# Optimization experiments

Measured on AMD Instinct MI355X. Metric: run time of the kernel, lower is better.

The kernel has to match this reference:

```python
import jax, jax.numpy as jnp
import numpy as np

B, N, D = 256, 131072, 256
TEMP = 0.05
EPS_SM = 1e-6
EPS_LOG = 1e-6
NUM_CLUSTERS = 1000


def _l2norm(x):
    return x / jnp.linalg.norm(x, axis=-1, keepdims=True)


def setup_inputs() -> dict:
    key = jax.random.key(0)
    k1, k2, k3, k4, k5 = jax.random.split(key, 5)
    # re-ID features are L2-normalized in practice; keeps exp(logits/temp) finite
    inputs = _l2norm(jax.random.normal(k1, (B, D), jnp.float32))
    indexes = jax.random.randint(k2, (B,), 0, N)
    labels = jax.random.randint(k3, (N,), 0, NUM_CLUSTERS)  # pseudo cluster ids buffer
    cluster_features = _l2norm(jax.random.normal(k4, (N, D), jnp.float32))
    instance_features = _l2norm(jax.random.normal(k5, (N, D), jnp.float32))
    return {
        "inputs": inputs,
        "cluster_features": cluster_features,
        "instance_features": instance_features,
        "indexes": indexes,
        "labels": labels,
    }


def reference(inputs, cluster_features, instance_features, indexes, labels):
    # targets = labels[indexes]
    targets = labels[indexes]
    # bank similarity GEMM, temperature scaling
    logits = jnp.matmul(inputs, cluster_features.T) / TEMP  # [B, N]
    # module's custom softmax: exp / (sum + eps)  (intentionally no max-subtract)
    exps = jnp.exp(logits)
    masked_sim = exps / (jnp.sum(exps, axis=1, keepdims=True) + EPS_SM)
    logp = jnp.log(masked_sim + EPS_LOG)
    # F.nll_loss: mean of -logp at target column
    loss = -jnp.mean(jnp.take_along_axis(logp, targets[:, None], axis=1))
    return loss
```

## Files before the change

### kernel.cpp

```cpp
#include <hip/hip_runtime.h>
#include <hip/hip_bf16.h>
#include <cstdint>

#define B_ 256
#define N_ 131072
#define D_ 256
#define INV_TEMP 20.0f
#define EPS_SM 1e-6f
#define EPS_LOG 1e-6f

#define TPB 512
#define BN 128
#define BK 64
#define TILES 4
#define LDB 72
#define BUFE (BN * LDB)
#define NSLOT 32
#define NBLK (N_ / (TILES * BN))

typedef __bf16 bf16_t;
typedef bf16_t bf16x8 __attribute__((ext_vector_type(8)));
typedef float f32x4 __attribute__((ext_vector_type(4)));

__device__ inline ushort f2bf(float f) {
  uint32_t u = __builtin_bit_cast(uint32_t, f);
  u += 0x7FFFu + ((u >> 16) & 1u);
  return (ushort)(u >> 16);
}

struct alignas(16) U8 { ushort u[8]; };

__global__ __launch_bounds__(TPB, 2)
void gemm_rowsum_fused(const float* __restrict__ inp, const float* __restrict__ cf,
                       const int* __restrict__ idx, const int* __restrict__ lab,
                       float* __restrict__ rowsum, unsigned* __restrict__ counter,
                       float* __restrict__ out) {
  __shared__ ushort smem[2 * BUFE];
  __shared__ unsigned done;
  const int tid  = threadIdx.x;
  const int wave = tid >> 6;
  const int lane = tid & 63;
  const int m15  = lane & 15;
  const int q    = lane >> 4;

  const size_t nbase = (size_t)blockIdx.x * (TILES * BN);
  const int brow = tid >> 2, bcg = tid & 3;
#define LDADDR(c) (cf + (nbase + (size_t)((c) >> 2) * BN + brow) * D_ + ((c) & 3) * BK + bcg * 16)

  float4 ldbuf[2][4];
#pragma unroll
  for (int i = 0; i < 4; ++i) ldbuf[0][i] = *(const float4*)(LDADDR(0) + i * 4);
#pragma unroll
  for (int i = 0; i < 4; ++i) ldbuf[1][i] = *(const float4*)(LDADDR(1) + i * 4);

  bf16x8 areg[8][2];
#pragma unroll
  for (int kc = 0; kc < 4; ++kc)
#pragma unroll
    for (int ks = 0; ks < 2; ++ks)
#pragma unroll
      for (int mb = 0; mb < 2; ++mb) {
        const float* s = inp + (wave * 32 + mb * 16 + m15) * D_ + kc * BK + ks * 32 + q * 8;
        const float4 v0 = *(const float4*)s;
        const float4 v1 = *(const float4*)(s + 4);
        U8 t;
        t.u[0] = f2bf(v0.x); t.u[1] = f2bf(v0.y); t.u[2] = f2bf(v0.z); t.u[3] = f2bf(v0.w);
        t.u[4] = f2bf(v1.x); t.u[5] = f2bf(v1.y); t.u[6] = f2bf(v1.z); t.u[7] = f2bf(v1.w);
        areg[kc * 2 + ks][mb] = __builtin_bit_cast(bf16x8, t);
      }

  f32x4 acc[2][8];
  float rs[2][4];
#pragma unroll
  for (int mb = 0; mb < 2; ++mb) {
#pragma unroll
    for (int nb = 0; nb < 8; ++nb) acc[mb][nb] = (f32x4){0.f, 0.f, 0.f, 0.f};
#pragma unroll
    for (int r = 0; r < 4; ++r) rs[mb][r] = 0.f;
  }

  {
    ushort* dst = &smem[brow * LDB + bcg * 16];
#pragma unroll
    for (int i = 0; i < 4; ++i) {
      const float4 v = ldbuf[0][i];
      U8 w;
      w.u[0] = f2bf(v.x); w.u[1] = f2bf(v.y); w.u[2] = f2bf(v.z); w.u[3] = f2bf(v.w);
      *(ushort4*)(dst + i * 4) = *(const ushort4*)&w.u[0];
    }
  }

#pragma unroll
  for (int c = 0; c < TILES * 4; ++c) {
    __syncthreads();
    if (c + 2 < TILES * 4) {
#pragma unroll
      for (int i = 0; i < 4; ++i) ldbuf[c & 1][i] = *(const float4*)(LDADDR(c + 2) + i * 4);
    }
    const ushort* bs = &smem[(c & 1) * BUFE];
#pragma unroll
    for (int ks = 0; ks < 2; ++ks) {
      bf16x8 bfr[8];
#pragma unroll
      for (int nb = 0; nb < 8; ++nb)
        bfr[nb] = __builtin_bit_cast(
            bf16x8, *(const uint4*)(&bs[(nb * 16 + m15) * LDB + ks * 32 + q * 8]));
#pragma unroll
      for (int mb = 0; mb < 2; ++mb)
#pragma unroll
        for (int nb = 0; nb < 8; ++nb)
          acc[mb][nb] = __builtin_amdgcn_mfma_f32_16x16x32_bf16(
              areg[(c & 3) * 2 + ks][mb], bfr[nb], acc[mb][nb], 0, 0, 0);
    }
    if ((c & 3) == 3) {
#pragma unroll
      for (int mb = 0; mb < 2; ++mb)
#pragma unroll
        for (int nb = 0; nb < 8; ++nb)
#pragma unroll
          for (int r = 0; r < 4; ++r)
            rs[mb][r] += __expf(acc[mb][nb][r] * INV_TEMP);
      if (c + 1 < TILES * 4) {
#pragma unroll
        for (int mb = 0; mb < 2; ++mb)
#pragma unroll
          for (int nb = 0; nb < 8; ++nb) acc[mb][nb] = (f32x4){0.f, 0.f, 0.f, 0.f};
      }
    }
    if (c + 1 < TILES * 4) {
      ushort* dst = &smem[((c + 1) & 1) * BUFE + brow * LDB + bcg * 16];
#pragma unroll
      for (int i = 0; i < 4; ++i) {
        const float4 v = ldbuf[(c + 1) & 1][i];
        U8 w;
        w.u[0] = f2bf(v.x); w.u[1] = f2bf(v.y); w.u[2] = f2bf(v.z); w.u[3] = f2bf(v.w);
        *(ushort4*)(dst + i * 4) = *(const ushort4*)&w.u[0];
      }
    }
  }

#pragma unroll
  for (int off = 8; off >= 1; off >>= 1)
#pragma unroll
    for (int mb = 0; mb < 2; ++mb)
#pragma unroll
      for (int r = 0; r < 4; ++r)
        rs[mb][r] += __shfl_xor(rs[mb][r], off, 64);

  if (m15 == 0) {
    float* slot = rowsum + (blockIdx.x & (NSLOT - 1)) * B_;
#pragma unroll
    for (int mb = 0; mb < 2; ++mb)
#pragma unroll
      for (int r = 0; r < 4; ++r)
        atomicAdd(&slot[wave * 32 + mb * 16 + q * 4 + r], rs[mb][r]);
  }
#undef LDADDR

  __syncthreads();
  if (tid == 0) {
    __threadfence();
    const unsigned prev = __hip_atomic_fetch_add(counter, 1u, __ATOMIC_ACQ_REL,
                                                 __HIP_MEMORY_SCOPE_AGENT);
    done = (prev == (unsigned)(gridDim.x - 1)) ? 1u : 0u;
  }
  __syncthreads();
  if (done) {
    __threadfence();
    float* red = (float*)smem;
    const int b = tid >> 1, part = tid & 1;
    const int t = lab[idx[b]];
    const float4* a4 = (const float4*)(inp + b * D_ + part * 128);
    const float4* c4 = (const float4*)(cf + (size_t)t * D_ + part * 128);
    float dot = 0.f;
#pragma unroll
    for (int i = 0; i < 32; ++i) {
      const float4 x = a4[i], y = c4[i];
      dot += x.x * y.x + x.y * y.y + x.z * y.z + x.w * y.w;
    }
    red[tid] = dot;
    __syncthreads();
    if (tid < 256) {
      const float d = red[2 * tid] + red[2 * tid + 1];
      float S = 0.f;
#pragma unroll
      for (int s = 0; s < NSLOT; ++s)
        S += __hip_atomic_load(&rowsum[s * B_ + tid], __ATOMIC_RELAXED,
                               __HIP_MEMORY_SCOPE_AGENT);
      red[512 + tid] = __logf(__expf(d * INV_TEMP) / (S + EPS_SM) + EPS_LOG);
    }
    __syncthreads();
    for (int off = 128; off >= 1; off >>= 1) {
      if (tid < off) red[512 + tid] += red[512 + tid + off];
      __syncthreads();
    }
    if (tid == 0) out[0] = -red[512] * (1.0f / 256.0f);
  }
}

extern "C" void kernel_launch(void* const* d_in, const int* in_sizes, int n_in,
                              void* d_out, int out_size, void* d_ws, size_t ws_size,
                              hipStream_t stream) {
  const float* inp = (const float*)d_in[0];
  const float* cf  = (const float*)d_in[1];
  const int* idx = (const int*)d_in[3];
  const int* lab = (const int*)d_in[4];
  float* out = (float*)d_out;
  float* rowsum = (float*)d_ws;
  unsigned* counter = (unsigned*)(rowsum + NSLOT * B_);

  hipMemsetAsync(d_ws, 0, (NSLOT * B_ + 16) * sizeof(float), stream);
  gemm_rowsum_fused<<<dim3(NBLK), dim3(TPB), 0, stream>>>(inp, cf, idx, lab,
                                                          rowsum, counter, out);
}
```

Before: 292.8 us.

## Shrink bank tile to 32 rows per chunk and stage input conversion via LDS

Cuts the per-chunk bank tile from 128 to 32 rows and gives each block 256 bank rows instead of 512, so the grid doubles to 512 blocks. Launch bounds rise to 4 blocks per CU, which needs the smaller accumulator footprint. The input matrix is now converted to bf16 with coalesced loads into shared memory and then read back into registers, where before each lane loaded it directly from global. The prefetch depth also changes to loads issued three chunks ahead. The aim is more occupancy and latency hiding on a memory-bound GEMM, at the cost of more barriers per unit of work, and only 4 MFMAs per ks step shared between those barriers.

```diff
diff --git a/kernel.cpp b/kernel.cpp
--- a/kernel.cpp
+++ b/kernel.cpp
@@ -10,13 +10,14 @@
 #define EPS_LOG 1e-6f
 
 #define TPB 512
-#define BN 128
+#define BROWS 256
+#define BN 32
 #define BK 64
-#define TILES 4
+#define NCHUNK 32
 #define LDB 72
 #define BUFE (BN * LDB)
 #define NSLOT 32
-#define NBLK (N_ / (TILES * BN))
+#define NBLK (N_ / BROWS)
 
 typedef __bf16 bf16_t;
 typedef bf16_t bf16x8 __attribute__((ext_vector_type(8)));
@@ -28,14 +29,12 @@
   return (ushort)(u >> 16);
 }
 
-struct alignas(16) U8 { ushort u[8]; };
-
-__global__ __launch_bounds__(TPB, 2)
+__global__ __launch_bounds__(TPB, 4)
 void gemm_rowsum_fused(const float* __restrict__ inp, const float* __restrict__ cf,
                        const int* __restrict__ idx, const int* __restrict__ lab,
                        float* __restrict__ rowsum, unsigned* __restrict__ counter,
                        float* __restrict__ out) {
-  __shared__ ushort smem[2 * BUFE];
+  __shared__ ushort smem[B_ * LDB];
   __shared__ unsigned done;
   const int tid  = threadIdx.x;
   const int wave = tid >> 6;
@@ -43,72 +42,67 @@
   const int m15  = lane & 15;
   const int q    = lane >> 4;
 
-  const size_t nbase = (size_t)blockIdx.x * (TILES * BN);
-  const int brow = tid >> 2, bcg = tid & 3;
-#define LDADDR(c) (cf + (nbase + (size_t)((c) >> 2) * BN + brow) * D_ + ((c) & 3) * BK + bcg * 16)
-
-  float4 ldbuf[2][4];
-#pragma unroll
-  for (int i = 0; i < 4; ++i) ldbuf[0][i] = *(const float4*)(LDADDR(0) + i * 4);
-#pragma unroll
-  for (int i = 0; i < 4; ++i) ldbuf[1][i] = *(const float4*)(LDADDR(1) + i * 4);
+  const size_t nbase = (size_t)blockIdx.x * BROWS;
+  const int brow = tid >> 4, bcg = tid & 15;
+#define LDADDR(c) (cf + (nbase + (size_t)((c) >> 2) * BN + brow) * D_ + ((c) & 3) * BK + bcg * 4)
+
+  float4 ldbuf[2];
+  ldbuf[0] = *(const float4*)LDADDR(0);
+  ldbuf[1] = *(const float4*)LDADDR(1);
 
   bf16x8 areg[8][2];
 #pragma unroll
-  for (int kc = 0; kc < 4; ++kc)
-#pragma unroll
-    for (int ks = 0; ks < 2; ++ks)
-#pragma unroll
-      for (int mb = 0; mb < 2; ++mb) {
-        const float* s = inp + (wave * 32 + mb * 16 + m15) * D_ + kc * BK + ks * 32 + q * 8;
-        const float4 v0 = *(const float4*)s;
-        const float4 v1 = *(const float4*)(s + 4);
-        U8 t;
-        t.u[0] = f2bf(v0.x); t.u[1] = f2bf(v0.y); t.u[2] = f2bf(v0.z); t.u[3] = f2bf(v0.w);
-        t.u[4] = f2bf(v1.x); t.u[5] = f2bf(v1.y); t.u[6] = f2bf(v1.z); t.u[7] = f2bf(v1.w);
-        areg[kc * 2 + ks][mb] = __builtin_bit_cast(bf16x8, t);
-      }
-
-  f32x4 acc[2][8];
+  for (int kc = 0; kc < 4; ++kc) {
+    const int row = tid >> 1, half = tid & 1;
+    const float* src = inp + row * D_ + kc * BK + half * 32;
+#pragma unroll
+    for (int i = 0; i < 8; ++i) {
+      const float4 v = *(const float4*)(src + i * 4);
+      ushort4 w = {f2bf(v.x), f2bf(v.y), f2bf(v.z), f2bf(v.w)};
+      *(ushort4*)(&smem[row * LDB + half * 32 + i * 4]) = w;
+    }
+    __syncthreads();
+#pragma unroll
+    for (int mb = 0; mb < 2; ++mb)
+#pragma unroll
+      for (int ks = 0; ks < 2; ++ks)
+        areg[kc * 2 + ks][mb] = __builtin_bit_cast(
+            bf16x8, *(const uint4*)(&smem[(wave * 32 + mb * 16 + m15) * LDB + ks * 32 + q * 8]));
+    __syncthreads();
+  }
+
+  f32x4 acc[2][2];
   float rs[2][4];
 #pragma unroll
   for (int mb = 0; mb < 2; ++mb) {
 #pragma unroll
-    for (int nb = 0; nb < 8; ++nb) acc[mb][nb] = (f32x4){0.f, 0.f, 0.f, 0.f};
+    for (int nb = 0; nb < 2; ++nb) acc[mb][nb] = (f32x4){0.f, 0.f, 0.f, 0.f};
 #pragma unroll
     for (int r = 0; r < 4; ++r) rs[mb][r] = 0.f;
   }
 
   {
-    ushort* dst = &smem[brow * LDB + bcg * 16];
-#pragma unroll
-    for (int i = 0; i < 4; ++i) {
-      const float4 v = ldbuf[0][i];
-      U8 w;
-      w.u[0] = f2bf(v.x); w.u[1] = f2bf(v.y); w.u[2] = f2bf(v.z); w.u[3] = f2bf(v.w);
-      *(ushort4*)(dst + i * 4) = *(const ushort4*)&w.u[0];
-    }
-  }
-
-#pragma unroll
-  for (int c = 0; c < TILES * 4; ++c) {
-    __syncthreads();
-    if (c + 2 < TILES * 4) {
-#pragma unroll
-      for (int i = 0; i < 4; ++i) ldbuf[c & 1][i] = *(const float4*)(LDADDR(c + 2) + i * 4);
-    }
+    const float4 v = ldbuf[0];
+    ushort4 w = {f2bf(v.x), f2bf(v.y), f2bf(v.z), f2bf(v.w)};
+    *(ushort4*)(&smem[brow * LDB + bcg * 4]) = w;
+  }
+  ldbuf[0] = *(const float4*)LDADDR(2);
+
+#pragma unroll
+  for (int c = 0; c < NCHUNK; ++c) {
+    __syncthreads();
     const ushort* bs = &smem[(c & 1) * BUFE];
 #pragma unroll
     for (int ks = 0; ks < 2; ++ks) {
-      bf16x8 bfr[8];
-#pragma unroll
-      for (int nb = 0; nb < 8; ++nb)
+      bf16x8 bfr[2];
+#pragma unroll
+      for (int nb = 0; nb < 2; ++nb)
         bfr[nb] = __builtin_bit_cast(
             bf16x8, *(const uint4*)(&bs[(nb * 16 + m15) * LDB + ks * 32 + q * 8]));
 #pragma unroll
       for (int mb = 0; mb < 2; ++mb)
 #pragma unroll
-        for (int nb = 0; nb < 8; ++nb)
+        for (int nb = 0; nb < 2; ++nb)
           acc[mb][nb] = __builtin_amdgcn_mfma_f32_16x16x32_bf16(
               areg[(c & 3) * 2 + ks][mb], bfr[nb], acc[mb][nb], 0, 0, 0);
     }
@@ -116,26 +110,24 @@
 #pragma unroll
       for (int mb = 0; mb < 2; ++mb)
 #pragma unroll
-        for (int nb = 0; nb < 8; ++nb)
+        for (int nb = 0; nb < 2; ++nb)
 #pragma unroll
           for (int r = 0; r < 4; ++r)
             rs[mb][r] += __expf(acc[mb][nb][r] * INV_TEMP);
-      if (c + 1 < TILES * 4) {
+      if (c + 1 < NCHUNK) {
 #pragma unroll
         for (int mb = 0; mb < 2; ++mb)
 #pragma unroll
-          for (int nb = 0; nb < 8; ++nb) acc[mb][nb] = (f32x4){0.f, 0.f, 0.f, 0.f};
+          for (int nb = 0; nb < 2; ++nb) acc[mb][nb] = (f32x4){0.f, 0.f, 0.f, 0.f};
       }
     }
-    if (c + 1 < TILES * 4) {
-      ushort* dst = &smem[((c + 1) & 1) * BUFE + brow * LDB + bcg * 16];
-#pragma unroll
-      for (int i = 0; i < 4; ++i) {
-        const float4 v = ldbuf[(c + 1) & 1][i];
-        U8 w;
-        w.u[0] = f2bf(v.x); w.u[1] = f2bf(v.y); w.u[2] = f2bf(v.z); w.u[3] = f2bf(v.w);
-        *(ushort4*)(dst + i * 4) = *(const ushort4*)&w.u[0];
-      }
+    if (c + 1 < NCHUNK) {
+      const float4 v = ldbuf[(c + 1) & 1];
+      ushort4 w = {f2bf(v.x), f2bf(v.y), f2bf(v.z), f2bf(v.w)};
+      *(ushort4*)(&smem[((c + 1) & 1) * BUFE + brow * LDB + bcg * 4]) = w;
+    }
+    if (c + 3 < NCHUNK) {
+      ldbuf[(c + 1) & 1] = *(const float4*)LDADDR(c + 3);
     }
   }
 
@@ -162,7 +154,7 @@
     __threadfence();
     const unsigned prev = __hip_atomic_fetch_add(counter, 1u, __ATOMIC_ACQ_REL,
                                                  __HIP_MEMORY_SCOPE_AGENT);
-    done = (prev == (unsigned)(gridDim.x - 1)) ? 1u : 0u;
+    done = (prev == (unsigned)(NBLK - 1)) ? 1u : 0u;
   }
   __syncthreads();
   if (done) {
```

New measurement: 325.1 us. +11.0%, slower.
